# Performance work log

Measured on AMD Instinct MI355X. Metric: run time of the kernel, lower is better.

Reference implementation:

```python
import jax, jax.numpy as jnp
import numpy as np

N = 100_000            # particles
E = 3_200_000          # edges (avg degree 32)
DIM = 3
H = 1.0                # kernel_radius
SIGMA = 3.0 / 359.0 / np.pi / H**3   # 3D quintic kernel normalization
RHO_REF = 1.0
P_REF = 100.0          # rho_ref * (10*u_ref)**2 / gamma, gamma=1
P_BG = 0.0             # p_bg_factor * p_ref
ETA0 = 0.01            # base_viscosity
EPS = 1e-8


def _qpows(d, p):
    q = d / H
    return (jnp.maximum(0.0, 1.0 - q) ** p,
            jnp.maximum(0.0, 2.0 - q) ** p,
            jnp.maximum(0.0, 3.0 - q) ** p)


def kernel_w(d):
    q1, q2, q3 = _qpows(d, 5)
    return SIGMA * (q3 - 6.0 * q2 + 15.0 * q1)


def kernel_grad_w(d):
    q1, q2, q3 = _qpows(d, 4)
    return (SIGMA / H) * (-5.0 * q3 + 30.0 * q2 - 75.0 * q1)


def setup_inputs() -> dict:
    key = jax.random.key(0)
    k1, k2, k3, k4 = jax.random.split(key, 4)
    r = jax.random.uniform(k1, (N, DIM), dtype=jnp.float32)   # positions in unit box
    v = jax.random.normal(k2, (N, DIM), dtype=jnp.float32)    # velocity history (last frame)
    i_s = jax.random.randint(k3, (E,), 0, N)                  # receivers
    j_s = jax.random.randint(k4, (E,), 0, N)                  # senders
    return {"r": r, "v": v, "i_s": i_s, "j_s": j_s}


def reference(r, v, i_s, j_s):
    n = r.shape[0]
    # --- per-edge gather + kernel ---
    dr = r[i_s] - r[j_s]                       # displacement_fn, [E,3]
    d = jnp.sqrt(jnp.sum(dr * dr, axis=-1))    # [E]
    w = kernel_w(d)
    # --- density summation (scatter) ---
    mass = jnp.ones((n,), r.dtype)
    rho = mass * jax.ops.segment_sum(w, i_s, num_segments=n)
    # Tait EoS, gamma=1
    p = P_REF * (rho / RHO_REF - 1.0) + P_BG
    eta = jnp.full((n,), ETA0, r.dtype)

    # --- per-edge acceleration (gather particle fields to edges) ---
    rho_i, rho_j = rho[i_s], rho[j_s]
    p_i, p_j = p[i_s], p[j_s]
    eta_i, eta_j = eta[i_s], eta[j_s]
    u_i, u_j = v[i_s], v[j_s]                  # u == v in _transform
    v_i, v_j = u_i, u_j

    eta_ij = 2.0 * eta_i * eta_j / (eta_i + eta_j + EPS)
    p_ij = (rho_j * p_i + rho_i * p_j) / (rho_i + rho_j)
    # ((m_i/rho_i)^2 + (m_j/rho_j)^2)/m_i with m == 1
    wvol = (1.0 / rho_i) ** 2 + (1.0 / rho_j) ** 2
    c = wvol * kernel_grad_w(d) / (d + EPS)    # [E]

    # transport stress A = (outer(rho_i*u_i, v_i-u_i) + outer(rho_j*u_j, v_j-u_j))/2, [E,3,3]
    A = 0.5 * (rho_i[:, None, None] * u_i[:, :, None] * (v_i - u_i)[:, None, :]
               + rho_j[:, None, None] * u_j[:, :, None] * (v_j - u_j)[:, None, :])
    Ar = jnp.einsum('eij,ej->ei', A, dr)

    a_eq_8 = c[:, None] * (-p_ij[:, None] * dr + Ar + eta_ij[:, None] * (u_i - u_j))
    p_bg_i = jnp.zeros_like(p_i)               # _transform passes zeros
    a_eq_13 = (c * p_bg_i)[:, None] * dr

    # --- scatter-reduce to particles ---
    dudt = jax.ops.segment_sum(a_eq_8, i_s, num_segments=n)   # [N,3]
    dvdt = jax.ops.segment_sum(a_eq_13, i_s, num_segments=n)  # [N,3]

    # pack state outputs: [rho, p, dudt(3), dvdt(3)] -> [N,8]
    return jnp.concatenate([rho[:, None], p[:, None], dudt, dvdt], axis=1)
```

## Files before the change

### kernel.cpp

```cpp
#include <hip/hip_runtime.h>
#include <math.h>

#ifndef M_PI
#define M_PI 3.14159265358979323846
#endif

static constexpr float kSigma = (float)(3.0 / 359.0 / M_PI);
static constexpr float kPRef  = 100.0f;
static constexpr float kEps   = 1e-8f;
static constexpr float kEta   = (float)(2.0 * 0.01 * 0.01 / (0.01 + 0.01 + 1e-8));

#define CHUNKH 4096
#define CHUNKS 8192
#define NSUB   4
#define BAT    8

__device__ __forceinline__ float pow5f(float t) { float t2 = t * t; return t2 * t2 * t; }
__device__ __forceinline__ float pow4f(float t) { float t2 = t * t; return t2 * t2; }

__global__ void k_pack(const float* __restrict__ r, float4* __restrict__ pos4, int n) {
    int i = blockIdx.x * blockDim.x + threadIdx.x;
    if (i >= n) return;
    pos4[i] = make_float4(r[3 * i], r[3 * i + 1], r[3 * i + 2], 0.f);
}

__global__ void k_hist(const int* __restrict__ i_s, int* __restrict__ ghist,
                       int nbAh, int nbins, int E, int shift) {
    __shared__ int h[512];
    int t = threadIdx.x, blk = blockIdx.x;
    for (int b = t; b < nbins; b += 256) h[b] = 0;
    __syncthreads();
    int base = blk * CHUNKH;
    int end = min(base + CHUNKH, E);
    for (int kb = base; kb < end; kb += 256 * 4) {
        int iv[4];
#pragma unroll
        for (int b = 0; b < 4; b++) {
            int k = kb + b * 256 + t;
            iv[b] = (k < end) ? i_s[k] : -1;
        }
#pragma unroll
        for (int b = 0; b < 4; b++)
            if (iv[b] >= 0) atomicAdd(&h[iv[b] >> shift], 1);
    }
    __syncthreads();
    for (int b = t; b < nbins; b += 256)
        ghist[b * nbAh + blk] = h[b];
}

__global__ void k_scan_block(const int* __restrict__ in, int* __restrict__ out,
                             int* __restrict__ bsum, int m) {
    __shared__ int s[256];
    int t = threadIdx.x;
    int i = blockIdx.x * 256 + t;
    int x = (i < m) ? in[i] : 0;
    s[t] = x;
    __syncthreads();
    for (int d = 1; d < 256; d <<= 1) {
        int v = (t >= d) ? s[t - d] : 0;
        __syncthreads();
        s[t] += v;
        __syncthreads();
    }
    if (i < m) out[i] = s[t] - x;
    if (t == 255) bsum[blockIdx.x] = s[255];
}

__global__ void k_scan_bsums(const int* __restrict__ bsum, int* __restrict__ bscan, int nb) {
    __shared__ int s[512];
    __shared__ int carry;
    int t = threadIdx.x;
    if (t == 0) carry = 0;
    __syncthreads();
    for (int base = 0; base < nb; base += 512) {
        int i = base + t;
        int x = (i < nb) ? bsum[i] : 0;
        s[t] = x;
        __syncthreads();
        for (int d = 1; d < 512; d <<= 1) {
            int v = (t >= d) ? s[t - d] : 0;
            __syncthreads();
            s[t] += v;
            __syncthreads();
        }
        if (i < nb) bscan[i] = s[t] - x + carry;
        __syncthreads();
        if (t == 511) carry += s[511];
        __syncthreads();
    }
}

__device__ __forceinline__ int scanned(const int* __restrict__ gscan,
                                       const int* __restrict__ bscan, int idx) {
    return gscan[idx] + bscan[idx >> 8];
}

__global__ void k_split(const int* __restrict__ i_s, const int* __restrict__ j_s,
                        const int* __restrict__ gscan, const int* __restrict__ bscan,
                        int* __restrict__ pairs, int nbAh, int nbins, int E,
                        int shift, int jbits) {
    __shared__ int cur[512];
    int t = threadIdx.x, blk = blockIdx.x;
    for (int b = t; b < nbins; b += 512)
        cur[b] = scanned(gscan, bscan, b * nbAh + 2 * blk);
    __syncthreads();
    int fmask = (1 << shift) - 1;
    int base = blk * CHUNKS;
    int end = min(base + CHUNKS, E);
    for (int kb = base; kb < end; kb += 512 * 4) {
        int iv[4], jv[4];
#pragma unroll
        for (int b = 0; b < 4; b++) {
            int k = kb + b * 512 + t;
            iv[b] = (k < end) ? i_s[k] : -1;
            jv[b] = (k < end) ? j_s[k] : 0;
        }
#pragma unroll
        for (int b = 0; b < 4; b++) {
            if (iv[b] < 0) continue;
            int pos = atomicAdd(&cur[iv[b] >> shift], 1);
            pairs[pos] = ((iv[b] & fmask) << jbits) | jv[b];
        }
    }
}

__global__ void k_rho_bin(const float4* __restrict__ pos4, const int* __restrict__ pairs,
                          const int* __restrict__ gscan, const int* __restrict__ bscan,
                          float* __restrict__ part_rho, int nbAh, int n, int E,
                          int shift, int jbits, int nbins) {
    __shared__ float srho[512];
    __shared__ float4 spos[512];
    __shared__ int sse[2];
    int bin = blockIdx.x >> 2, sub = blockIdx.x & (NSUB - 1);
    int t = threadIdx.x;
    int slots = 1 << shift;
    int lo = bin << shift;
    for (int s0 = t; s0 < slots; s0 += 256) {
        srho[s0] = 0.f;
        int ii = lo + s0;
        spos[s0] = (ii < n) ? pos4[ii] : make_float4(0.f, 0.f, 0.f, 0.f);
    }
    if (t == 0) {
        sse[0] = scanned(gscan, bscan, bin * nbAh);
        sse[1] = (bin + 1 < nbins) ? scanned(gscan, bscan, (bin + 1) * nbAh) : E;
    }
    __syncthreads();
    int s = sse[0], len = sse[1] - sse[0];
    int k0 = s + (int)((long)len * sub / NSUB);
    int k1 = s + (int)((long)len * (sub + 1) / NSUB);
    int jm = (1 << jbits) - 1;
    for (int kb = k0; kb < k1; kb += 256 * BAT) {
        int pr[BAT];
#pragma unroll
        for (int b = 0; b < BAT; b++) {
            int k = kb + b * 256 + t;
            pr[b] = (k < k1) ? pairs[k] : -1;
        }
        float4 rj[BAT];
#pragma unroll
        for (int b = 0; b < BAT; b++)
            if (pr[b] >= 0) rj[b] = pos4[pr[b] & jm];
#pragma unroll
        for (int b = 0; b < BAT; b++) {
            if (pr[b] < 0) continue;
            int slot = pr[b] >> jbits;
            float4 ri = spos[slot];
            float dx = ri.x - rj[b].x, dy = ri.y - rj[b].y, dz = ri.z - rj[b].z;
            float d = sqrtf(dx * dx + dy * dy + dz * dz);
            float t1 = fmaxf(1.f - d, 0.f);
            float t2 = fmaxf(2.f - d, 0.f);
            float t3 = fmaxf(3.f - d, 0.f);
            float w = kSigma * (pow5f(t3) - 6.f * pow5f(t2) + 15.f * pow5f(t1));
            atomicAdd(&srho[slot], w);
        }
    }
    __syncthreads();
    for (int s0 = t; s0 < slots; s0 += 256) {
        int ii = lo + s0;
        if (ii < n) part_rho[(size_t)sub * n + ii] = srho[s0];
    }
}

__global__ void k_reduce_rho(const float* __restrict__ part_rho,
                             const float4* __restrict__ pos4, const float* __restrict__ v,
                             float4* __restrict__ pv8, float* __restrict__ out, int n) {
    int i = blockIdx.x * blockDim.x + threadIdx.x;
    if (i >= n) return;
    float rh = 0.f;
    for (int s = 0; s < NSUB; s++) rh += part_rho[(size_t)s * n + i];
    float pp = kPRef * (rh - 1.0f);
    float4 sp = pos4[i];
    pv8[2 * i]     = make_float4(sp.x, sp.y, sp.z, rh);
    pv8[2 * i + 1] = make_float4(v[3 * i], v[3 * i + 1], v[3 * i + 2], pp);
    float* o = out + (size_t)i * 8;
    o[0] = rh;
    o[1] = pp;
    o[5] = 0.f; o[6] = 0.f; o[7] = 0.f;
}

__global__ void k_acc_bin(const float4* __restrict__ pv8, const int* __restrict__ pairs,
                          const int* __restrict__ gscan, const int* __restrict__ bscan,
                          float4* __restrict__ part_acc4, int nbAh, int n, int E,
                          int shift, int jbits, int nbins) {
    __shared__ float sax[512], say[512], saz[512];
    __shared__ float4 sab[1024];
    __shared__ int sse[2];
    int bin = blockIdx.x >> 2, sub = blockIdx.x & (NSUB - 1);
    int t = threadIdx.x;
    int slots = 1 << shift;
    int lo = bin << shift;
    for (int s0 = t; s0 < slots; s0 += 256) { sax[s0] = 0.f; say[s0] = 0.f; saz[s0] = 0.f; }
    for (int q = t; q < 2 * slots; q += 256) {
        int gi = 2 * lo + q;
        sab[q] = (gi < 2 * n) ? pv8[gi] : make_float4(1.f, 1.f, 1.f, 1.f);
    }
    if (t == 0) {
        sse[0] = scanned(gscan, bscan, bin * nbAh);
        sse[1] = (bin + 1 < nbins) ? scanned(gscan, bscan, (bin + 1) * nbAh) : E;
    }
    __syncthreads();
    int s = sse[0], len = sse[1] - sse[0];
    int k0 = s + (int)((long)len * sub / NSUB);
    int k1 = s + (int)((long)len * (sub + 1) / NSUB);
    int jm = (1 << jbits) - 1;
    for (int kb = k0; kb < k1; kb += 256 * BAT) {
        int pr[BAT];
#pragma unroll
        for (int b = 0; b < BAT; b++) {
            int k = kb + b * 256 + t;
            pr[b] = (k < k1) ? pairs[k] : -1;
        }
        float4 aj[BAT], bj[BAT];
#pragma unroll
        for (int b = 0; b < BAT; b++) {
            if (pr[b] >= 0) {
                int j = pr[b] & jm;
                aj[b] = pv8[2 * j];
                bj[b] = pv8[2 * j + 1];
            }
        }
#pragma unroll
        for (int b = 0; b < BAT; b++) {
            if (pr[b] < 0) continue;
            int slot = pr[b] >> jbits;
            float4 ai = sab[2 * slot];
            float4 bi = sab[2 * slot + 1];
            float rho_i = ai.w, p_i = bi.w;
            float rho_j = aj[b].w, p_j = bj[b].w;
            float dx = ai.x - aj[b].x, dy = ai.y - aj[b].y, dz = ai.z - aj[b].z;
            float d = sqrtf(dx * dx + dy * dy + dz * dz);
            float t1 = fmaxf(1.f - d, 0.f);
            float t2 = fmaxf(2.f - d, 0.f);
            float t3 = fmaxf(3.f - d, 0.f);
            float gw = kSigma * (-5.f * pow4f(t3) + 30.f * pow4f(t2) - 75.f * pow4f(t1));
            float inv_i = 1.0f / rho_i, inv_j = 1.0f / rho_j;
            float c = (inv_i * inv_i + inv_j * inv_j) * gw / (d + kEps);
            float p_ij = (rho_j * p_i + rho_i * p_j) / (rho_i + rho_j);
            atomicAdd(&sax[slot], c * (kEta * (bi.x - bj[b].x) - p_ij * dx));
            atomicAdd(&say[slot], c * (kEta * (bi.y - bj[b].y) - p_ij * dy));
            atomicAdd(&saz[slot], c * (kEta * (bi.z - bj[b].z) - p_ij * dz));
        }
    }
    __syncthreads();
    for (int s0 = t; s0 < slots; s0 += 256) {
        int ii = lo + s0;
        if (ii < n)
            part_acc4[(size_t)sub * n + ii] = make_float4(sax[s0], say[s0], saz[s0], 0.f);
    }
}

__global__ void k_reduce_acc(const float4* __restrict__ part_acc4,
                             float* __restrict__ out, int n) {
    int i = blockIdx.x * blockDim.x + threadIdx.x;
    if (i >= n) return;
    float ax = 0.f, ay = 0.f, az = 0.f;
    for (int s = 0; s < NSUB; s++) {
        float4 p = part_acc4[(size_t)s * n + i];
        ax += p.x; ay += p.y; az += p.z;
    }
    float* o = out + (size_t)i * 8 + 2;
    o[0] = ax; o[1] = ay; o[2] = az;
}

static inline char* wcarve(char*& ws, size_t bytes) {
    char* p = ws;
    ws += (bytes + 255) & ~(size_t)255;
    return p;
}

extern "C" void kernel_launch(void* const* d_in, const int* in_sizes, int n_in,
                              void* d_out, int out_size, void* d_ws, size_t ws_size,
                              hipStream_t stream) {
    const float* r = (const float*)d_in[0];
    const float* v = (const float*)d_in[1];
    const int* i_s = (const int*)d_in[2];
    const int* j_s = (const int*)d_in[3];
    int n = in_sizes[0] / 3;
    int E = in_sizes[2];
    float* out = (float*)d_out;

    int shift = 8;
    int nbins = ((n - 1) >> shift) + 1;
    while (nbins > 512) { shift++; nbins = ((n - 1) >> shift) + 1; }
    int jbits = 1;
    while ((1 << jbits) < n) jbits++;

    int nbAh = (E + CHUNKH - 1) / CHUNKH;
    int nbAs = (E + CHUNKS - 1) / CHUNKS;
    int m = nbins * nbAh;
    int nb2 = (m + 255) / 256;

    char* ws = (char*)d_ws;
    float4* pos4     = (float4*)wcarve(ws, (size_t)n * 16);
    float4* pv8      = (float4*)wcarve(ws, (size_t)n * 32);
    int*    ghist    = (int*)wcarve(ws, (size_t)m * 4);
    int*    gscan    = (int*)wcarve(ws, (size_t)m * 4);
    int*    bsum     = (int*)wcarve(ws, (size_t)nb2 * 4);
    int*    bscan    = (int*)wcarve(ws, (size_t)nb2 * 4);
    int*    pairs    = (int*)wcarve(ws, (size_t)E * 4);
    float*  part_rho = (float*)wcarve(ws, (size_t)NSUB * n * 4);
    float4* part_acc4= (float4*)wcarve(ws, (size_t)NSUB * n * 16);

    const int bs = 256;
    int gn = (n + bs - 1) / bs;

    k_pack<<<gn, bs, 0, stream>>>(r, pos4, n);
    k_hist<<<nbAh, 256, 0, stream>>>(i_s, ghist, nbAh, nbins, E, shift);
    k_scan_block<<<nb2, 256, 0, stream>>>(ghist, gscan, bsum, m);
    k_scan_bsums<<<1, 512, 0, stream>>>(bsum, bscan, nb2);
    k_split<<<nbAs, 512, 0, stream>>>(i_s, j_s, gscan, bscan, pairs, nbAh, nbins, E, shift, jbits);
    k_rho_bin<<<nbins * NSUB, 256, 0, stream>>>(pos4, pairs, gscan, bscan, part_rho, nbAh, n, E, shift, jbits, nbins);
    k_reduce_rho<<<gn, bs, 0, stream>>>(part_rho, pos4, v, pv8, out, n);
    k_acc_bin<<<nbins * NSUB, 256, 0, stream>>>(pv8, pairs, gscan, bscan, part_acc4, nbAh, n, E, shift, jbits, nbins);
    k_reduce_acc<<<gn, bs, 0, stream>>>(part_acc4, out, n);
}
```

Baseline: 221.1 us.

## Stage binned pairs in LDS, cache per-edge geometry in fp16, slim acc gather

```diff
diff --git a/kernel.cpp b/kernel.cpp
--- a/kernel.cpp
+++ b/kernel.cpp
@@ -10,10 +10,11 @@
 static constexpr float kEps   = 1e-8f;
 static constexpr float kEta   = (float)(2.0 * 0.01 * 0.01 / (0.01 + 0.01 + 1e-8));
 
-#define CHUNKH 4096
-#define CHUNKS 8192
-#define NSUB   4
-#define BAT    8
+#define CHUNK 4096
+#define NSUB  4
+#define BAT   4
+
+typedef _Float16 hf4 __attribute__((ext_vector_type(4)));
 
 __device__ __forceinline__ float pow5f(float t) { float t2 = t * t; return t2 * t2 * t; }
 __device__ __forceinline__ float pow4f(float t) { float t2 = t * t; return t2 * t2; }
@@ -25,13 +26,13 @@
 }
 
 __global__ void k_hist(const int* __restrict__ i_s, int* __restrict__ ghist,
-                       int nbAh, int nbins, int E, int shift) {
+                       int nbA, int nbins, int E, int shift) {
     __shared__ int h[512];
     int t = threadIdx.x, blk = blockIdx.x;
     for (int b = t; b < nbins; b += 256) h[b] = 0;
     __syncthreads();
-    int base = blk * CHUNKH;
-    int end = min(base + CHUNKH, E);
+    int base = blk * CHUNK;
+    int end = min(base + CHUNK, E);
     for (int kb = base; kb < end; kb += 256 * 4) {
         int iv[4];
 #pragma unroll
@@ -45,7 +46,7 @@
     }
     __syncthreads();
     for (int b = t; b < nbins; b += 256)
-        ghist[b * nbAh + blk] = h[b];
+        ghist[b * nbA + blk] = h[b];
 }
 
 __global__ void k_scan_block(const int* __restrict__ in, int* __restrict__ out,
@@ -96,73 +97,95 @@
 }
 
 __global__ void k_split(const int* __restrict__ i_s, const int* __restrict__ j_s,
-                        const int* __restrict__ gscan, const int* __restrict__ bscan,
-                        int* __restrict__ pairs, int nbAh, int nbins, int E,
-                        int shift, int jbits) {
-    __shared__ int cur[512];
+                        const int* __restrict__ ghist, const int* __restrict__ gscan,
+                        const int* __restrict__ bscan, int* __restrict__ pairs,
+                        int nbA, int nbins, int E, int shift, int jbits) {
+    __shared__ int lofs[512];
+    __shared__ int ldelta[512];
+    __shared__ int stage[CHUNK];
+    __shared__ unsigned short binof[CHUNK];
     int t = threadIdx.x, blk = blockIdx.x;
-    for (int b = t; b < nbins; b += 512)
-        cur[b] = scanned(gscan, bscan, b * nbAh + 2 * blk);
-    __syncthreads();
+    int base = blk * CHUNK;
+    int end = min(base + CHUNK, E);
+    int cnt = end - base;
+
+    int h0 = (t < nbins) ? ghist[t * nbA + blk] : 0;
+    int h1 = (t + 256 < nbins) ? ghist[(t + 256) * nbA + blk] : 0;
+    lofs[t] = h0;
+    lofs[t + 256] = h1;
+    __syncthreads();
+    for (int d = 1; d < 512; d <<= 1) {
+        int v0 = (t >= d) ? lofs[t - d] : 0;
+        int v1 = ((t + 256) >= d) ? lofs[t + 256 - d] : 0;
+        __syncthreads();
+        lofs[t] += v0;
+        lofs[t + 256] += v1;
+        __syncthreads();
+    }
+    int e0 = lofs[t] - h0;
+    int e1 = lofs[t + 256] - h1;
+    __syncthreads();
+    lofs[t] = e0;
+    lofs[t + 256] = e1;
+    if (t < nbins) ldelta[t] = scanned(gscan, bscan, t * nbA + blk) - e0;
+    if (t + 256 < nbins) ldelta[t + 256] = scanned(gscan, bscan, (t + 256) * nbA + blk) - e1;
+    __syncthreads();
+
     int fmask = (1 << shift) - 1;
-    int base = blk * CHUNKS;
-    int end = min(base + CHUNKS, E);
-    for (int kb = base; kb < end; kb += 512 * 4) {
+    for (int kb = base; kb < end; kb += 256 * 4) {
         int iv[4], jv[4];
 #pragma unroll
         for (int b = 0; b < 4; b++) {
-            int k = kb + b * 512 + t;
+            int k = kb + b * 256 + t;
             iv[b] = (k < end) ? i_s[k] : -1;
             jv[b] = (k < end) ? j_s[k] : 0;
         }
 #pragma unroll
         for (int b = 0; b < 4; b++) {
             if (iv[b] < 0) continue;
-            int pos = atomicAdd(&cur[iv[b] >> shift], 1);
-            pairs[pos] = ((iv[b] & fmask) << jbits) | jv[b];
-        }
-    }
+            int bin = iv[b] >> shift;
+            int pos = atomicAdd(&lofs[bin], 1);
+            stage[pos] = ((iv[b] & fmask) << jbits) | jv[b];
+            binof[pos] = (unsigned short)bin;
+        }
+    }
+    __syncthreads();
+    for (int x = t; x < cnt; x += 256)
+        pairs[x + ldelta[binof[x]]] = stage[x];
 }
 
 __global__ void k_rho_bin(const float4* __restrict__ pos4, const int* __restrict__ pairs,
                           const int* __restrict__ gscan, const int* __restrict__ bscan,
-                          float* __restrict__ part_rho, int nbAh, int n, int E,
-                          int shift, int jbits, int nbins) {
-    __shared__ float srho[512];
-    __shared__ float4 spos[512];
+                          float* __restrict__ part_rho, hf4* __restrict__ aux,
+                          int nbA, int n, int E, int shift, int jbits, int nbins) {
+    __shared__ float srho[256];
+    __shared__ float4 spos[256];
     __shared__ int sse[2];
     int bin = blockIdx.x >> 2, sub = blockIdx.x & (NSUB - 1);
     int t = threadIdx.x;
-    int slots = 1 << shift;
     int lo = bin << shift;
-    for (int s0 = t; s0 < slots; s0 += 256) {
-        srho[s0] = 0.f;
-        int ii = lo + s0;
-        spos[s0] = (ii < n) ? pos4[ii] : make_float4(0.f, 0.f, 0.f, 0.f);
-    }
+    srho[t] = 0.f;
+    int ii = lo + t;
+    spos[t] = (ii < n) ? pos4[ii] : make_float4(0.f, 0.f, 0.f, 0.f);
     if (t == 0) {
-        sse[0] = scanned(gscan, bscan, bin * nbAh);
-        sse[1] = (bin + 1 < nbins) ? scanned(gscan, bscan, (bin + 1) * nbAh) : E;
+        sse[0] = scanned(gscan, bscan, bin * nbA);
+        sse[1] = (bin + 1 < nbins) ? scanned(gscan, bscan, (bin + 1) * nbA) : E;
     }
     __syncthreads();
     int s = sse[0], len = sse[1] - sse[0];
     int k0 = s + (int)((long)len * sub / NSUB);
     int k1 = s + (int)((long)len * (sub + 1) / NSUB);
     int jm = (1 << jbits) - 1;
-    for (int kb = k0; kb < k1; kb += 256 * BAT) {
+    int kb = k0;
+    for (; kb + 256 * BAT <= k1; kb += 256 * BAT) {
         int pr[BAT];
 #pragma unroll
+        for (int b = 0; b < BAT; b++) pr[b] = pairs[kb + b * 256 + t];
+        float4 rj[BAT];
+#pragma unroll
+        for (int b = 0; b < BAT; b++) rj[b] = pos4[pr[b] & jm];
+#pragma unroll
         for (int b = 0; b < BAT; b++) {
-            int k = kb + b * 256 + t;
-            pr[b] = (k < k1) ? pairs[k] : -1;
-        }
-        float4 rj[BAT];
-#pragma unroll
-        for (int b = 0; b < BAT; b++)
-            if (pr[b] >= 0) rj[b] = pos4[pr[b] & jm];
-#pragma unroll
-        for (int b = 0; b < BAT; b++) {
-            if (pr[b] < 0) continue;
             int slot = pr[b] >> jbits;
             float4 ri = spos[slot];
             float dx = ri.x - rj[b].x, dy = ri.y - rj[b].y, dz = ri.z - rj[b].z;
@@ -172,83 +195,93 @@
             float t3 = fmaxf(3.f - d, 0.f);
             float w = kSigma * (pow5f(t3) - 6.f * pow5f(t2) + 15.f * pow5f(t1));
             atomicAdd(&srho[slot], w);
-        }
-    }
-    __syncthreads();
-    for (int s0 = t; s0 < slots; s0 += 256) {
-        int ii = lo + s0;
-        if (ii < n) part_rho[(size_t)sub * n + ii] = srho[s0];
-    }
+            hf4 h;
+            h.x = (_Float16)dx; h.y = (_Float16)dy;
+            h.z = (_Float16)dz; h.w = (_Float16)d;
+            aux[kb + b * 256 + t] = h;
+        }
+    }
+    for (int k = kb + t; k < k1; k += 256) {
+        int pr = pairs[k];
+        int slot = pr >> jbits;
+        float4 rj = pos4[pr & jm];
+        float4 ri = spos[slot];
+        float dx = ri.x - rj.x, dy = ri.y - rj.y, dz = ri.z - rj.z;
+        float d = sqrtf(dx * dx + dy * dy + dz * dz);
+        float t1 = fmaxf(1.f - d, 0.f);
+        float t2 = fmaxf(2.f - d, 0.f);
+        float t3 = fmaxf(3.f - d, 0.f);
+        float w = kSigma * (pow5f(t3) - 6.f * pow5f(t2) + 15.f * pow5f(t1));
+        atomicAdd(&srho[slot], w);
+        hf4 h;
+        h.x = (_Float16)dx; h.y = (_Float16)dy;
+        h.z = (_Float16)dz; h.w = (_Float16)d;
+        aux[k] = h;
+    }
+    __syncthreads();
+    if (ii < n) part_rho[(size_t)sub * n + ii] = srho[t];
 }
 
 __global__ void k_reduce_rho(const float* __restrict__ part_rho,
-                             const float4* __restrict__ pos4, const float* __restrict__ v,
-                             float4* __restrict__ pv8, float* __restrict__ out, int n) {
+                             const float* __restrict__ v,
+                             float4* __restrict__ vp4, float* __restrict__ out, int n) {
     int i = blockIdx.x * blockDim.x + threadIdx.x;
     if (i >= n) return;
     float rh = 0.f;
     for (int s = 0; s < NSUB; s++) rh += part_rho[(size_t)s * n + i];
     float pp = kPRef * (rh - 1.0f);
-    float4 sp = pos4[i];
-    pv8[2 * i]     = make_float4(sp.x, sp.y, sp.z, rh);
-    pv8[2 * i + 1] = make_float4(v[3 * i], v[3 * i + 1], v[3 * i + 2], pp);
+    vp4[i] = make_float4(v[3 * i], v[3 * i + 1], v[3 * i + 2], pp);
     float* o = out + (size_t)i * 8;
     o[0] = rh;
     o[1] = pp;
     o[5] = 0.f; o[6] = 0.f; o[7] = 0.f;
 }
 
-__global__ void k_acc_bin(const float4* __restrict__ pv8, const int* __restrict__ pairs,
+__global__ void k_acc_bin(const float4* __restrict__ vp4, const int* __restrict__ pairs,
+                          const hf4* __restrict__ aux,
                           const int* __restrict__ gscan, const int* __restrict__ bscan,
-                          float4* __restrict__ part_acc4, int nbAh, int n, int E,
+                          float4* __restrict__ part_acc4, int nbA, int n, int E,
                           int shift, int jbits, int nbins) {
-    __shared__ float sax[512], say[512], saz[512];
-    __shared__ float4 sab[1024];
+    __shared__ float sax[256], say[256], saz[256];
+    __shared__ float4 svp[256];
     __shared__ int sse[2];
     int bin = blockIdx.x >> 2, sub = blockIdx.x & (NSUB - 1);
     int t = threadIdx.x;
-    int slots = 1 << shift;
     int lo = bin << shift;
-    for (int s0 = t; s0 < slots; s0 += 256) { sax[s0] = 0.f; say[s0] = 0.f; saz[s0] = 0.f; }
-    for (int q = t; q < 2 * slots; q += 256) {
-        int gi = 2 * lo + q;
-        sab[q] = (gi < 2 * n) ? pv8[gi] : make_float4(1.f, 1.f, 1.f, 1.f);
-    }
+    sax[t] = 0.f; say[t] = 0.f; saz[t] = 0.f;
+    int ii = lo + t;
+    svp[t] = (ii < n) ? vp4[ii] : make_float4(0.f, 0.f, 0.f, 0.f);
     if (t == 0) {
-        sse[0] = scanned(gscan, bscan, bin * nbAh);
-        sse[1] = (bin + 1 < nbins) ? scanned(gscan, bscan, (bin + 1) * nbAh) : E;
+        sse[0] = scanned(gscan, bscan, bin * nbA);
+        sse[1] = (bin + 1 < nbins) ? scanned(gscan, bscan, (bin + 1) * nbA) : E;
     }
     __syncthreads();
     int s = sse[0], len = sse[1] - sse[0];
     int k0 = s + (int)((long)len * sub / NSUB);
     int k1 = s + (int)((long)len * (sub + 1) / NSUB);
     int jm = (1 << jbits) - 1;
-    for (int kb = k0; kb < k1; kb += 256 * BAT) {
+    int kb = k0;
+    for (; kb + 256 * BAT <= k1; kb += 256 * BAT) {
         int pr[BAT];
+        hf4 hx[BAT];
 #pragma unroll
         for (int b = 0; b < BAT; b++) {
             int k = kb + b * 256 + t;
-            pr[b] = (k < k1) ? pairs[k] : -1;
-        }
-        float4 aj[BAT], bj[BAT];
+            pr[b] = pairs[k];
+            hx[b] = aux[k];
+        }
+        float4 vj[BAT];
+#pragma unroll
+        for (int b = 0; b < BAT; b++) vj[b] = vp4[pr[b] & jm];
 #pragma unroll
         for (int b = 0; b < BAT; b++) {
-            if (pr[b] >= 0) {
-                int j = pr[b] & jm;
-                aj[b] = pv8[2 * j];
-                bj[b] = pv8[2 * j + 1];
-            }
-        }
-#pragma unroll
-        for (int b = 0; b < BAT; b++) {
-            if (pr[b] < 0) continue;
             int slot = pr[b] >> jbits;
-            float4 ai = sab[2 * slot];
-            float4 bi = sab[2 * slot + 1];
-            float rho_i = ai.w, p_i = bi.w;
-            float rho_j = aj[b].w, p_j = bj[b].w;
-            float dx = ai.x - aj[b].x, dy = ai.y - aj[b].y, dz = ai.z - aj[b].z;
-            float d = sqrtf(dx * dx + dy * dy + dz * dz);
+            float4 bi = svp[slot];
+            float p_i = bi.w, p_j = vj[b].w;
+            float rho_i = p_i * 0.01f + 1.0f;
+            float rho_j = p_j * 0.01f + 1.0f;
+            float dx = (float)hx[b].x, dy = (float)hx[b].y, dz = (float)hx[b].z;
+            float d = (float)hx[b].w;
             float t1 = fmaxf(1.f - d, 0.f);
             float t2 = fmaxf(2.f - d, 0.f);
             float t3 = fmaxf(3.f - d, 0.f);
@@ -256,17 +289,36 @@
             float inv_i = 1.0f / rho_i, inv_j = 1.0f / rho_j;
             float c = (inv_i * inv_i + inv_j * inv_j) * gw / (d + kEps);
             float p_ij = (rho_j * p_i + rho_i * p_j) / (rho_i + rho_j);
-            atomicAdd(&sax[slot], c * (kEta * (bi.x - bj[b].x) - p_ij * dx));
-            atomicAdd(&say[slot], c * (kEta * (bi.y - bj[b].y) - p_ij * dy));
-            atomicAdd(&saz[slot], c * (kEta * (bi.z - bj[b].z) - p_ij * dz));
-        }
-    }
-    __syncthreads();
-    for (int s0 = t; s0 < slots; s0 += 256) {
-        int ii = lo + s0;
-        if (ii < n)
-            part_acc4[(size_t)sub * n + ii] = make_float4(sax[s0], say[s0], saz[s0], 0.f);
-    }
+            atomicAdd(&sax[slot], c * (kEta * (bi.x - vj[b].x) - p_ij * dx));
+            atomicAdd(&say[slot], c * (kEta * (bi.y - vj[b].y) - p_ij * dy));
+            atomicAdd(&saz[slot], c * (kEta * (bi.z - vj[b].z) - p_ij * dz));
+        }
+    }
+    for (int k = kb + t; k < k1; k += 256) {
+        int pr = pairs[k];
+        hf4 hx = aux[k];
+        int slot = pr >> jbits;
+        float4 vj = vp4[pr & jm];
+        float4 bi = svp[slot];
+        float p_i = bi.w, p_j = vj.w;
+        float rho_i = p_i * 0.01f + 1.0f;
+        float rho_j = p_j * 0.01f + 1.0f;
+        float dx = (float)hx.x, dy = (float)hx.y, dz = (float)hx.z;
+        float d = (float)hx.w;
+        float t1 = fmaxf(1.f - d, 0.f);
+        float t2 = fmaxf(2.f - d, 0.f);
+        float t3 = fmaxf(3.f - d, 0.f);
+        float gw = kSigma * (-5.f * pow4f(t3) + 30.f * pow4f(t2) - 75.f * pow4f(t1));
+        float inv_i = 1.0f / rho_i, inv_j = 1.0f / rho_j;
+        float c = (inv_i * inv_i + inv_j * inv_j) * gw / (d + kEps);
+        float p_ij = (rho_j * p_i + rho_i * p_j) / (rho_i + rho_j);
+        atomicAdd(&sax[slot], c * (kEta * (bi.x - vj.x) - p_ij * dx));
+        atomicAdd(&say[slot], c * (kEta * (bi.y - vj.y) - p_ij * dy));
+        atomicAdd(&saz[slot], c * (kEta * (bi.z - vj.z) - p_ij * dz));
+    }
+    __syncthreads();
+    if (ii < n)
+        part_acc4[(size_t)sub * n + ii] = make_float4(sax[t], say[t], saz[t], 0.f);
 }
 
 __global__ void k_reduce_acc(const float4* __restrict__ part_acc4,
@@ -305,19 +357,19 @@
     int jbits = 1;
     while ((1 << jbits) < n) jbits++;
 
-    int nbAh = (E + CHUNKH - 1) / CHUNKH;
-    int nbAs = (E + CHUNKS - 1) / CHUNKS;
-    int m = nbins * nbAh;
+    int nbA = (E + CHUNK - 1) / CHUNK;
+    int m = nbins * nbA;
     int nb2 = (m + 255) / 256;
 
     char* ws = (char*)d_ws;
     float4* pos4     = (float4*)wcarve(ws, (size_t)n * 16);
-    float4* pv8      = (float4*)wcarve(ws, (size_t)n * 32);
+    float4* vp4      = (float4*)wcarve(ws, (size_t)n * 16);
     int*    ghist    = (int*)wcarve(ws, (size_t)m * 4);
     int*    gscan    = (int*)wcarve(ws, (size_t)m * 4);
     int*    bsum     = (int*)wcarve(ws, (size_t)nb2 * 4);
     int*    bscan    = (int*)wcarve(ws, (size_t)nb2 * 4);
     int*    pairs    = (int*)wcarve(ws, (size_t)E * 4);
+    hf4*    aux      = (hf4*)wcarve(ws, (size_t)E * 8);
     float*  part_rho = (float*)wcarve(ws, (size_t)NSUB * n * 4);
     float4* part_acc4= (float4*)wcarve(ws, (size_t)NSUB * n * 16);
 
@@ -325,12 +377,12 @@
     int gn = (n + bs - 1) / bs;
 
     k_pack<<<gn, bs, 0, stream>>>(r, pos4, n);
-    k_hist<<<nbAh, 256, 0, stream>>>(i_s, ghist, nbAh, nbins, E, shift);
+    k_hist<<<nbA, 256, 0, stream>>>(i_s, ghist, nbA, nbins, E, shift);
     k_scan_block<<<nb2, 256, 0, stream>>>(ghist, gscan, bsum, m);
     k_scan_bsums<<<1, 512, 0, stream>>>(bsum, bscan, nb2);
-    k_split<<<nbAs, 512, 0, stream>>>(i_s, j_s, gscan, bscan, pairs, nbAh, nbins, E, shift, jbits);
-    k_rho_bin<<<nbins * NSUB, 256, 0, stream>>>(pos4, pairs, gscan, bscan, part_rho, nbAh, n, E, shift, jbits, nbins);
-    k_reduce_rho<<<gn, bs, 0, stream>>>(part_rho, pos4, v, pv8, out, n);
-    k_acc_bin<<<nbins * NSUB, 256, 0, stream>>>(pv8, pairs, gscan, bscan, part_acc4, nbAh, n, E, shift, jbits, nbins);
+    k_split<<<nbA, 256, 0, stream>>>(i_s, j_s, ghist, gscan, bscan, pairs, nbA, nbins, E, shift, jbits);
+    k_rho_bin<<<nbins * NSUB, 256, 0, stream>>>(pos4, pairs, gscan, bscan, part_rho, aux, nbA, n, E, shift, jbits, nbins);
+    k_reduce_rho<<<gn, bs, 0, stream>>>(part_rho, v, vp4, out, n);
+    k_acc_bin<<<nbins * NSUB, 256, 0, stream>>>(vp4, pairs, aux, gscan, bscan, part_acc4, nbA, n, E, shift, jbits, nbins);
     k_reduce_acc<<<gn, bs, 0, stream>>>(part_acc4, out, n);
 }
```

Result: faster. 199.8 us (-9.6%).

## Bucket edges by receiver and sender blocks, stage splits in LDS, store fp16 particle data

Applied to the files above, without the earlier changes.

```diff
diff --git a/kernel.cpp b/kernel.cpp
--- a/kernel.cpp
+++ b/kernel.cpp
@@ -10,51 +10,67 @@
 static constexpr float kEps   = 1e-8f;
 static constexpr float kEta   = (float)(2.0 * 0.01 * 0.01 / (0.01 + 0.01 + 1e-8));
 
-#define CHUNKH 4096
-#define CHUNKS 8192
-#define NSUB   4
-#define BAT    8
+#define CHUNK 4096
+#define SI    10
+#define NBMAX 5120
+#define JG    4
+
+typedef _Float16 hf4 __attribute__((ext_vector_type(4)));
+typedef _Float16 hf8 __attribute__((ext_vector_type(8)));
 
 __device__ __forceinline__ float pow5f(float t) { float t2 = t * t; return t2 * t2 * t; }
 __device__ __forceinline__ float pow4f(float t) { float t2 = t * t; return t2 * t2; }
 
-__global__ void k_pack(const float* __restrict__ r, float4* __restrict__ pos4, int n) {
+__device__ __forceinline__ int scanned(const int* __restrict__ gscan,
+                                       const int* __restrict__ bscan, int idx) {
+    return gscan[idx] + bscan[idx >> 10];
+}
+
+__global__ void k_pack(const float* __restrict__ r, hf4* __restrict__ pos_h, int n) {
     int i = blockIdx.x * blockDim.x + threadIdx.x;
     if (i >= n) return;
-    pos4[i] = make_float4(r[3 * i], r[3 * i + 1], r[3 * i + 2], 0.f);
-}
-
-__global__ void k_hist(const int* __restrict__ i_s, int* __restrict__ ghist,
-                       int nbAh, int nbins, int E, int shift) {
-    __shared__ int h[512];
+    hf4 h;
+    h.x = (_Float16)r[3 * i]; h.y = (_Float16)r[3 * i + 1];
+    h.z = (_Float16)r[3 * i + 2]; h.w = (_Float16)0.f;
+    pos_h[i] = h;
+}
+
+__global__ void k_hist(const int* __restrict__ i_s, const int* __restrict__ j_s,
+                       int* __restrict__ ghist, int nbA, int nbuck, int NJ,
+                       int E, int sj) {
+    __shared__ int h[NBMAX];
     int t = threadIdx.x, blk = blockIdx.x;
-    for (int b = t; b < nbins; b += 256) h[b] = 0;
-    __syncthreads();
-    int base = blk * CHUNKH;
-    int end = min(base + CHUNKH, E);
+    for (int b = t; b < nbuck; b += 256) h[b] = 0;
+    __syncthreads();
+    int base = blk * CHUNK;
+    int end = min(base + CHUNK, E);
     for (int kb = base; kb < end; kb += 256 * 4) {
-        int iv[4];
+        int bv[4];
 #pragma unroll
         for (int b = 0; b < 4; b++) {
             int k = kb + b * 256 + t;
-            iv[b] = (k < end) ? i_s[k] : -1;
+            bv[b] = (k < end) ? ((i_s[k] >> SI) * NJ + (j_s[k] >> sj)) : -1;
         }
 #pragma unroll
         for (int b = 0; b < 4; b++)
-            if (iv[b] >= 0) atomicAdd(&h[iv[b] >> shift], 1);
-    }
-    __syncthreads();
-    for (int b = t; b < nbins; b += 256)
-        ghist[b * nbAh + blk] = h[b];
+            if (bv[b] >= 0) atomicAdd(&h[bv[b]], 1);
+    }
+    __syncthreads();
+    for (int b = t; b < nbuck; b += 256)
+        ghist[b * nbA + blk] = h[b];
 }
 
 __global__ void k_scan_block(const int* __restrict__ in, int* __restrict__ out,
                              int* __restrict__ bsum, int m) {
     __shared__ int s[256];
     int t = threadIdx.x;
-    int i = blockIdx.x * 256 + t;
-    int x = (i < m) ? in[i] : 0;
-    s[t] = x;
+    int base = blockIdx.x * 1024 + 4 * t;
+    int x0 = (base + 0 < m) ? in[base + 0] : 0;
+    int x1 = (base + 1 < m) ? in[base + 1] : 0;
+    int x2 = (base + 2 < m) ? in[base + 2] : 0;
+    int x3 = (base + 3 < m) ? in[base + 3] : 0;
+    int ts = x0 + x1 + x2 + x3;
+    s[t] = ts;
     __syncthreads();
     for (int d = 1; d < 256; d <<= 1) {
         int v = (t >= d) ? s[t - d] : 0;
@@ -62,7 +78,11 @@
         s[t] += v;
         __syncthreads();
     }
-    if (i < m) out[i] = s[t] - x;
+    int excl = s[t] - ts;
+    if (base + 0 < m) out[base + 0] = excl;
+    if (base + 1 < m) out[base + 1] = excl + x0;
+    if (base + 2 < m) out[base + 2] = excl + x0 + x1;
+    if (base + 3 < m) out[base + 3] = excl + x0 + x1 + x2;
     if (t == 255) bsum[blockIdx.x] = s[255];
 }
 
@@ -90,165 +110,175 @@
     }
 }
 
-__device__ __forceinline__ int scanned(const int* __restrict__ gscan,
-                                       const int* __restrict__ bscan, int idx) {
-    return gscan[idx] + bscan[idx >> 8];
-}
-
 __global__ void k_split(const int* __restrict__ i_s, const int* __restrict__ j_s,
-                        const int* __restrict__ gscan, const int* __restrict__ bscan,
-                        int* __restrict__ pairs, int nbAh, int nbins, int E,
-                        int shift, int jbits) {
-    __shared__ int cur[512];
+                        const int* __restrict__ ghist, const int* __restrict__ gscan,
+                        const int* __restrict__ bscan, int* __restrict__ pairs,
+                        int nbA, int nbuck, int NJ, int E, int sj, int jbits) {
+    __shared__ int lofs[NBMAX];
+    __shared__ int ldelta[NBMAX];
+    __shared__ int stage[CHUNK];
+    __shared__ unsigned short sbuck[CHUNK];
+    __shared__ int s[256];
+    __shared__ int carry;
     int t = threadIdx.x, blk = blockIdx.x;
-    for (int b = t; b < nbins; b += 512)
-        cur[b] = scanned(gscan, bscan, b * nbAh + 2 * blk);
-    __syncthreads();
-    int fmask = (1 << shift) - 1;
-    int base = blk * CHUNKS;
-    int end = min(base + CHUNKS, E);
-    for (int kb = base; kb < end; kb += 512 * 4) {
+    int base = blk * CHUNK;
+    int end = min(base + CHUNK, E);
+    int cnt = end - base;
+
+    if (t == 0) carry = 0;
+    __syncthreads();
+    for (int c = 0; c < nbuck; c += 256) {
+        int b = c + t;
+        int x = (b < nbuck) ? ghist[b * nbA + blk] : 0;
+        s[t] = x;
+        __syncthreads();
+        for (int d = 1; d < 256; d <<= 1) {
+            int v = (t >= d) ? s[t - d] : 0;
+            __syncthreads();
+            s[t] += v;
+            __syncthreads();
+        }
+        if (b < nbuck) {
+            int excl = s[t] - x + carry;
+            lofs[b] = excl;
+            ldelta[b] = scanned(gscan, bscan, b * nbA + blk) - excl;
+        }
+        __syncthreads();
+        if (t == 255) carry += s[255];
+        __syncthreads();
+    }
+
+    int smask = (1 << SI) - 1;
+    for (int kb = base; kb < end; kb += 256 * 4) {
         int iv[4], jv[4];
 #pragma unroll
         for (int b = 0; b < 4; b++) {
-            int k = kb + b * 512 + t;
+            int k = kb + b * 256 + t;
             iv[b] = (k < end) ? i_s[k] : -1;
             jv[b] = (k < end) ? j_s[k] : 0;
         }
 #pragma unroll
         for (int b = 0; b < 4; b++) {
             if (iv[b] < 0) continue;
-            int pos = atomicAdd(&cur[iv[b] >> shift], 1);
-            pairs[pos] = ((iv[b] & fmask) << jbits) | jv[b];
-        }
-    }
-}
-
-__global__ void k_rho_bin(const float4* __restrict__ pos4, const int* __restrict__ pairs,
-                          const int* __restrict__ gscan, const int* __restrict__ bscan,
-                          float* __restrict__ part_rho, int nbAh, int n, int E,
-                          int shift, int jbits, int nbins) {
-    __shared__ float srho[512];
-    __shared__ float4 spos[512];
+            int bk = (iv[b] >> SI) * NJ + (jv[b] >> sj);
+            int pos = atomicAdd(&lofs[bk], 1);
+            stage[pos] = ((iv[b] & smask) << jbits) | jv[b];
+            sbuck[pos] = (unsigned short)bk;
+        }
+    }
+    __syncthreads();
+    for (int x = t; x < cnt; x += 256)
+        pairs[x + ldelta[sbuck[x]]] = stage[x];
+}
+
+__global__ void k_rho(const hf4* __restrict__ pos_h, const int* __restrict__ pairs,
+                      const int* __restrict__ gscan, const int* __restrict__ bscan,
+                      float* __restrict__ part_rho, int nbA, int n, int E,
+                      int NJ, int jbits, int m) {
+    __shared__ hf4 spos[1024];
+    __shared__ float srho[1024];
     __shared__ int sse[2];
-    int bin = blockIdx.x >> 2, sub = blockIdx.x & (NSUB - 1);
-    int t = threadIdx.x;
-    int slots = 1 << shift;
-    int lo = bin << shift;
-    for (int s0 = t; s0 < slots; s0 += 256) {
+    int blk = blockIdx.x, t = threadIdx.x;
+    int ib = blk / NJ, jb = blk - ib * NJ;
+    int lo = ib << SI;
+    for (int s0 = t; s0 < 1024; s0 += 256) {
         srho[s0] = 0.f;
-        int ii = lo + s0;
-        spos[s0] = (ii < n) ? pos4[ii] : make_float4(0.f, 0.f, 0.f, 0.f);
+        int gi = lo + s0;
+        hf4 z; z.x = (_Float16)0.f; z.y = (_Float16)0.f; z.z = (_Float16)0.f; z.w = (_Float16)0.f;
+        spos[s0] = (gi < n) ? pos_h[gi] : z;
     }
     if (t == 0) {
-        sse[0] = scanned(gscan, bscan, bin * nbAh);
-        sse[1] = (bin + 1 < nbins) ? scanned(gscan, bscan, (bin + 1) * nbAh) : E;
-    }
-    __syncthreads();
-    int s = sse[0], len = sse[1] - sse[0];
-    int k0 = s + (int)((long)len * sub / NSUB);
-    int k1 = s + (int)((long)len * (sub + 1) / NSUB);
+        sse[0] = scanned(gscan, bscan, blk * nbA);
+        int i1 = (blk + 1) * nbA;
+        sse[1] = (i1 < m) ? scanned(gscan, bscan, i1) : E;
+    }
+    __syncthreads();
+    int s = sse[0], e = sse[1];
     int jm = (1 << jbits) - 1;
-    for (int kb = k0; kb < k1; kb += 256 * BAT) {
-        int pr[BAT];
-#pragma unroll
-        for (int b = 0; b < BAT; b++) {
-            int k = kb + b * 256 + t;
-            pr[b] = (k < k1) ? pairs[k] : -1;
-        }
-        float4 rj[BAT];
-#pragma unroll
-        for (int b = 0; b < BAT; b++)
-            if (pr[b] >= 0) rj[b] = pos4[pr[b] & jm];
-#pragma unroll
-        for (int b = 0; b < BAT; b++) {
-            if (pr[b] < 0) continue;
-            int slot = pr[b] >> jbits;
-            float4 ri = spos[slot];
-            float dx = ri.x - rj[b].x, dy = ri.y - rj[b].y, dz = ri.z - rj[b].z;
-            float d = sqrtf(dx * dx + dy * dy + dz * dz);
-            float t1 = fmaxf(1.f - d, 0.f);
-            float t2 = fmaxf(2.f - d, 0.f);
-            float t3 = fmaxf(3.f - d, 0.f);
-            float w = kSigma * (pow5f(t3) - 6.f * pow5f(t2) + 15.f * pow5f(t1));
-            atomicAdd(&srho[slot], w);
-        }
-    }
-    __syncthreads();
-    for (int s0 = t; s0 < slots; s0 += 256) {
-        int ii = lo + s0;
-        if (ii < n) part_rho[(size_t)sub * n + ii] = srho[s0];
+    for (int k = s + t; k < e; k += 256) {
+        int pr = pairs[k];
+        int slot = pr >> jbits, j = pr & jm;
+        hf4 pj = pos_h[j];
+        hf4 pi = spos[slot];
+        float dx = (float)pi.x - (float)pj.x;
+        float dy = (float)pi.y - (float)pj.y;
+        float dz = (float)pi.z - (float)pj.z;
+        float d = sqrtf(dx * dx + dy * dy + dz * dz);
+        float t1 = fmaxf(1.f - d, 0.f);
+        float t2 = fmaxf(2.f - d, 0.f);
+        float t3 = fmaxf(3.f - d, 0.f);
+        float w = kSigma * (pow5f(t3) - 6.f * pow5f(t2) + 15.f * pow5f(t1));
+        atomicAdd(&srho[slot], w);
+    }
+    __syncthreads();
+    for (int s0 = t; s0 < 1024; s0 += 256) {
+        int gi = lo + s0;
+        if (gi < n) part_rho[(size_t)jb * n + gi] = srho[s0];
     }
 }
 
 __global__ void k_reduce_rho(const float* __restrict__ part_rho,
-                             const float4* __restrict__ pos4, const float* __restrict__ v,
-                             float4* __restrict__ pv8, float* __restrict__ out, int n) {
+                             const hf4* __restrict__ pos_h, const float* __restrict__ v,
+                             hf8* __restrict__ pv16, float* __restrict__ out,
+                             int n, int NJ) {
     int i = blockIdx.x * blockDim.x + threadIdx.x;
     if (i >= n) return;
     float rh = 0.f;
-    for (int s = 0; s < NSUB; s++) rh += part_rho[(size_t)s * n + i];
+    for (int s = 0; s < NJ; s++) rh += part_rho[(size_t)s * n + i];
     float pp = kPRef * (rh - 1.0f);
-    float4 sp = pos4[i];
-    pv8[2 * i]     = make_float4(sp.x, sp.y, sp.z, rh);
-    pv8[2 * i + 1] = make_float4(v[3 * i], v[3 * i + 1], v[3 * i + 2], pp);
+    hf4 ph = pos_h[i];
+    hf8 rec;
+    rec[0] = ph.x; rec[1] = ph.y; rec[2] = ph.z; rec[3] = (_Float16)0.f;
+    rec[4] = (_Float16)v[3 * i]; rec[5] = (_Float16)v[3 * i + 1];
+    rec[6] = (_Float16)v[3 * i + 2]; rec[7] = (_Float16)pp;
+    pv16[i] = rec;
     float* o = out + (size_t)i * 8;
     o[0] = rh;
     o[1] = pp;
     o[5] = 0.f; o[6] = 0.f; o[7] = 0.f;
 }
 
-__global__ void k_acc_bin(const float4* __restrict__ pv8, const int* __restrict__ pairs,
-                          const int* __restrict__ gscan, const int* __restrict__ bscan,
-                          float4* __restrict__ part_acc4, int nbAh, int n, int E,
-                          int shift, int jbits, int nbins) {
-    __shared__ float sax[512], say[512], saz[512];
-    __shared__ float4 sab[1024];
-    __shared__ int sse[2];
-    int bin = blockIdx.x >> 2, sub = blockIdx.x & (NSUB - 1);
-    int t = threadIdx.x;
-    int slots = 1 << shift;
-    int lo = bin << shift;
-    for (int s0 = t; s0 < slots; s0 += 256) { sax[s0] = 0.f; say[s0] = 0.f; saz[s0] = 0.f; }
-    for (int q = t; q < 2 * slots; q += 256) {
-        int gi = 2 * lo + q;
-        sab[q] = (gi < 2 * n) ? pv8[gi] : make_float4(1.f, 1.f, 1.f, 1.f);
-    }
-    if (t == 0) {
-        sse[0] = scanned(gscan, bscan, bin * nbAh);
-        sse[1] = (bin + 1 < nbins) ? scanned(gscan, bscan, (bin + 1) * nbAh) : E;
-    }
-    __syncthreads();
-    int s = sse[0], len = sse[1] - sse[0];
-    int k0 = s + (int)((long)len * sub / NSUB);
-    int k1 = s + (int)((long)len * (sub + 1) / NSUB);
+__global__ void k_acc(const hf8* __restrict__ pv16, const int* __restrict__ pairs,
+                      const int* __restrict__ gscan, const int* __restrict__ bscan,
+                      float4* __restrict__ part_acc4, int nbA, int n, int E,
+                      int NJ, int NG, int jbits, int m) {
+    __shared__ hf8 spv[1024];
+    __shared__ float sax[1024], say[1024], saz[1024];
+    int blk = blockIdx.x, t = threadIdx.x;
+    int ib = blk / NG, jg = blk - ib * NG;
+    int lo = ib << SI;
+    for (int s0 = t; s0 < 1024; s0 += 256) {
+        sax[s0] = 0.f; say[s0] = 0.f; saz[s0] = 0.f;
+        int gi = lo + s0;
+        if (gi < n) spv[s0] = pv16[gi];
+        else {
+            hf8 z;
+#pragma unroll
+            for (int q = 0; q < 8; q++) z[q] = (_Float16)0.f;
+            spv[s0] = z;
+        }
+    }
+    __syncthreads();
     int jm = (1 << jbits) - 1;
-    for (int kb = k0; kb < k1; kb += 256 * BAT) {
-        int pr[BAT];
-#pragma unroll
-        for (int b = 0; b < BAT; b++) {
-            int k = kb + b * 256 + t;
-            pr[b] = (k < k1) ? pairs[k] : -1;
-        }
-        float4 aj[BAT], bj[BAT];
-#pragma unroll
-        for (int b = 0; b < BAT; b++) {
-            if (pr[b] >= 0) {
-                int j = pr[b] & jm;
-                aj[b] = pv8[2 * j];
-                bj[b] = pv8[2 * j + 1];
-            }
-        }
-#pragma unroll
-        for (int b = 0; b < BAT; b++) {
-            if (pr[b] < 0) continue;
-            int slot = pr[b] >> jbits;
-            float4 ai = sab[2 * slot];
-            float4 bi = sab[2 * slot + 1];
-            float rho_i = ai.w, p_i = bi.w;
-            float rho_j = aj[b].w, p_j = bj[b].w;
-            float dx = ai.x - aj[b].x, dy = ai.y - aj[b].y, dz = ai.z - aj[b].z;
+    for (int ph = 0; ph < JG; ph++) {
+        int jb = jg * JG + ph;
+        if (jb >= NJ) break;
+        int b = ib * NJ + jb;
+        int s = scanned(gscan, bscan, b * nbA);
+        int i1 = (b + 1) * nbA;
+        int e = (i1 < m) ? scanned(gscan, bscan, i1) : E;
+        for (int k = s + t; k < e; k += 256) {
+            int pr = pairs[k];
+            int slot = pr >> jbits, j = pr & jm;
+            hf8 pvj = pv16[j];
+            hf8 pvi = spv[slot];
+            float dx = (float)pvi[0] - (float)pvj[0];
+            float dy = (float)pvi[1] - (float)pvj[1];
+            float dz = (float)pvi[2] - (float)pvj[2];
             float d = sqrtf(dx * dx + dy * dy + dz * dz);
+            float p_i = (float)pvi[7], p_j = (float)pvj[7];
+            float rho_i = p_i * 0.01f + 1.0f;
+            float rho_j = p_j * 0.01f + 1.0f;
             float t1 = fmaxf(1.f - d, 0.f);
             float t2 = fmaxf(2.f - d, 0.f);
             float t3 = fmaxf(3.f - d, 0.f);
@@ -256,25 +286,28 @@
             float inv_i = 1.0f / rho_i, inv_j = 1.0f / rho_j;
             float c = (inv_i * inv_i + inv_j * inv_j) * gw / (d + kEps);
             float p_ij = (rho_j * p_i + rho_i * p_j) / (rho_i + rho_j);
-            atomicAdd(&sax[slot], c * (kEta * (bi.x - bj[b].x) - p_ij * dx));
-            atomicAdd(&say[slot], c * (kEta * (bi.y - bj[b].y) - p_ij * dy));
-            atomicAdd(&saz[slot], c * (kEta * (bi.z - bj[b].z) - p_ij * dz));
-        }
-    }
-    __syncthreads();
-    for (int s0 = t; s0 < slots; s0 += 256) {
-        int ii = lo + s0;
-        if (ii < n)
-            part_acc4[(size_t)sub * n + ii] = make_float4(sax[s0], say[s0], saz[s0], 0.f);
+            float ux = (float)pvi[4] - (float)pvj[4];
+            float uy = (float)pvi[5] - (float)pvj[5];
+            float uz = (float)pvi[6] - (float)pvj[6];
+            atomicAdd(&sax[slot], c * (kEta * ux - p_ij * dx));
+            atomicAdd(&say[slot], c * (kEta * uy - p_ij * dy));
+            atomicAdd(&saz[slot], c * (kEta * uz - p_ij * dz));
+        }
+    }
+    __syncthreads();
+    for (int s0 = t; s0 < 1024; s0 += 256) {
+        int gi = lo + s0;
+        if (gi < n)
+            part_acc4[(size_t)jg * n + gi] = make_float4(sax[s0], say[s0], saz[s0], 0.f);
     }
 }
 
 __global__ void k_reduce_acc(const float4* __restrict__ part_acc4,
-                             float* __restrict__ out, int n) {
+                             float* __restrict__ out, int n, int NG) {
     int i = blockIdx.x * blockDim.x + threadIdx.x;
     if (i >= n) return;
     float ax = 0.f, ay = 0.f, az = 0.f;
-    for (int s = 0; s < NSUB; s++) {
+    for (int s = 0; s < NG; s++) {
         float4 p = part_acc4[(size_t)s * n + i];
         ax += p.x; ay += p.y; az += p.z;
     }
@@ -299,38 +332,40 @@
     int E = in_sizes[2];
     float* out = (float*)d_out;
 
-    int shift = 8;
-    int nbins = ((n - 1) >> shift) + 1;
-    while (nbins > 512) { shift++; nbins = ((n - 1) >> shift) + 1; }
+    int NI = ((n - 1) >> SI) + 1;
+    int sj = 11;
+    int NJ = ((n - 1) >> sj) + 1;
+    while (NI * NJ > NBMAX) { sj++; NJ = ((n - 1) >> sj) + 1; }
+    int nbuck = NI * NJ;
+    int NG = (NJ + JG - 1) / JG;
     int jbits = 1;
     while ((1 << jbits) < n) jbits++;
 
-    int nbAh = (E + CHUNKH - 1) / CHUNKH;
-    int nbAs = (E + CHUNKS - 1) / CHUNKS;
-    int m = nbins * nbAh;
-    int nb2 = (m + 255) / 256;
+    int nbA = (E + CHUNK - 1) / CHUNK;
+    int m = nbuck * nbA;
+    int nb2 = (m + 1023) / 1024;
 
     char* ws = (char*)d_ws;
-    float4* pos4     = (float4*)wcarve(ws, (size_t)n * 16);
-    float4* pv8      = (float4*)wcarve(ws, (size_t)n * 32);
+    hf4*    pos_h    = (hf4*)wcarve(ws, (size_t)n * 8);
+    hf8*    pv16     = (hf8*)wcarve(ws, (size_t)n * 16);
     int*    ghist    = (int*)wcarve(ws, (size_t)m * 4);
     int*    gscan    = (int*)wcarve(ws, (size_t)m * 4);
     int*    bsum     = (int*)wcarve(ws, (size_t)nb2 * 4);
     int*    bscan    = (int*)wcarve(ws, (size_t)nb2 * 4);
     int*    pairs    = (int*)wcarve(ws, (size_t)E * 4);
-    float*  part_rho = (float*)wcarve(ws, (size_t)NSUB * n * 4);
-    float4* part_acc4= (float4*)wcarve(ws, (size_t)NSUB * n * 16);
+    float*  part_rho = (float*)wcarve(ws, (size_t)NJ * n * 4);
+    float4* part_acc4= (float4*)wcarve(ws, (size_t)NG * n * 16);
 
     const int bs = 256;
     int gn = (n + bs - 1) / bs;
 
-    k_pack<<<gn, bs, 0, stream>>>(r, pos4, n);
-    k_hist<<<nbAh, 256, 0, stream>>>(i_s, ghist, nbAh, nbins, E, shift);
+    k_pack<<<gn, bs, 0, stream>>>(r, pos_h, n);
+    k_hist<<<nbA, 256, 0, stream>>>(i_s, j_s, ghist, nbA, nbuck, NJ, E, sj);
     k_scan_block<<<nb2, 256, 0, stream>>>(ghist, gscan, bsum, m);
     k_scan_bsums<<<1, 512, 0, stream>>>(bsum, bscan, nb2);
-    k_split<<<nbAs, 512, 0, stream>>>(i_s, j_s, gscan, bscan, pairs, nbAh, nbins, E, shift, jbits);
-    k_rho_bin<<<nbins * NSUB, 256, 0, stream>>>(pos4, pairs, gscan, bscan, part_rho, nbAh, n, E, shift, jbits, nbins);
-    k_reduce_rho<<<gn, bs, 0, stream>>>(part_rho, pos4, v, pv8, out, n);
-    k_acc_bin<<<nbins * NSUB, 256, 0, stream>>>(pv8, pairs, gscan, bscan, part_acc4, nbAh, n, E, shift, jbits, nbins);
-    k_reduce_acc<<<gn, bs, 0, stream>>>(part_acc4, out, n);
-}
+    k_split<<<nbA, 256, 0, stream>>>(i_s, j_s, ghist, gscan, bscan, pairs, nbA, nbuck, NJ, E, sj, jbits);
+    k_rho<<<nbuck, 256, 0, stream>>>(pos_h, pairs, gscan, bscan, part_rho, nbA, n, E, NJ, jbits, m);
+    k_reduce_rho<<<gn, bs, 0, stream>>>(part_rho, pos_h, v, pv16, out, n, NJ);
+    k_acc<<<NI * NG, 256, 0, stream>>>(pv16, pairs, gscan, bscan, part_acc4, nbA, n, E, NJ, NG, jbits, m);
+    k_reduce_acc<<<gn, bs, 0, stream>>>(part_acc4, out, n, NG);
+}
```

After: 348.9 us. 1.58x slower.
